# Kernel tuning notes

Measured on AMD Instinct MI355X. Metric: run time of the kernel, lower is better.

Reference implementation:

```python
import jax, jax.numpy as jnp
import numpy as np

D_MODEL = 1024
N_HEADS = 16
D_HEAD = D_MODEL // N_HEADS
MODES = 32


def setup_inputs() -> dict:
    key = jax.random.key(0)
    ks = jax.random.split(key, 7)
    B, L = 4, 4096
    s = 1.0 / np.sqrt(D_MODEL)
    return {
        "q_in": jax.random.normal(ks[0], (B, L, D_MODEL), dtype=jnp.float32),
        "Wv": jax.random.uniform(ks[1], (D_MODEL, D_MODEL), jnp.float32, -s, s),
        "bv": jax.random.uniform(ks[2], (D_MODEL,), jnp.float32, -s, s),
        "Wo": jax.random.uniform(ks[3], (D_MODEL, D_MODEL), jnp.float32, -s, s),
        "bo": jax.random.uniform(ks[4], (D_MODEL,), jnp.float32, -s, s),
        "w_real": jax.random.normal(ks[5], (N_HEADS, MODES, D_HEAD), dtype=jnp.float32) * 0.02,
        "w_imag": jax.random.normal(ks[6], (N_HEADS, MODES, D_HEAD), dtype=jnp.float32) * 0.02,
    }


def reference(q_in, Wv, bv, Wo, bo, w_real, w_imag):
    B, L, dm = q_in.shape
    # v projection -> [B, H, L, Dh]
    v = (q_in @ Wv.T + bv).reshape(B, L, N_HEADS, D_HEAD).transpose(0, 2, 1, 3)
    # rFFT over time axis; keep only lowest MODES frequencies
    v_ft = jnp.fft.rfft(v, axis=2)                      # [B, H, L//2+1, Dh] complex
    w = (w_real + 1j * w_imag)[None]                    # [1, H, MODES, Dh]
    out_ft = v_ft[:, :, :MODES, :] * w                  # truncated spectrum
    # irfft zero-pads the truncated spectrum up to n//2+1 (== torch's zeros_like + slice-assign)
    out = jnp.fft.irfft(out_ft, n=L, axis=2)            # [B, H, L, Dh]
    out = out.transpose(0, 2, 1, 3).reshape(B, L, dm)
    return out @ Wo.T + bo
```

## Files before the change

### kernel.cpp

```cpp
#include <hip/hip_runtime.h>
#include <math.h>


typedef __attribute__((ext_vector_type(8))) short bf16x8;
typedef __attribute__((ext_vector_type(8))) unsigned short ushort8;
typedef __attribute__((ext_vector_type(4))) float f32x4;

__device__ __forceinline__ unsigned short f2bf(float x) {
    union { float f; unsigned int u; } c; c.f = x;
    unsigned int u = c.u + 0x7FFFu + ((c.u >> 16) & 1u);
    return (unsigned short)(u >> 16);
}

__global__ __launch_bounds__(256) void k_init(unsigned short* __restrict__ F,
                                              unsigned short* __restrict__ G,
                                              float* __restrict__ A) {
    int idx = blockIdx.x * 256 + threadIdx.x;
    const float w0 = 1.5339807878856412e-3f;
    {
        int j = idx >> 12, t = idx & 4095, k = j >> 1;
        int r = (k * t) & 4095;
        float s, c; sincosf((float)r * w0, &s, &c);
        F[idx] = f2bf((j & 1) ? -s : c);
    }
    {
        int j = idx & 63, k = j >> 1;
        int t = idx >> 6;
        int r = (k * t) & 4095;
        float s, c; sincosf((float)r * w0, &s, &c);
        float ck = (k == 0) ? (1.0f / 4096.0f) : (2.0f / 4096.0f);
        float v = (j & 1) ? ((k == 0) ? 0.0f : -ck * s) : ck * c;
        G[idx] = f2bf(v);
    }
    A[idx] = 0.0f;
}

__global__ __launch_bounds__(64) void k_dft_fwd(const float* __restrict__ q,
                                                const unsigned short* __restrict__ F,
                                                float* __restrict__ A) {
    __shared__ __align__(16) unsigned short Ft[64 * 40];
    __shared__ __align__(16) unsigned short qT[32 * 40];
    int blk = blockIdx.x;
    int kp = blk & 15, nt = (blk >> 4) & 31, b = blk >> 9;
    int n0 = nt * 32, t0 = kp * 256;
    int lane = threadIdx.x;
    int lm = lane & 15, q4 = lane >> 4;
    int nn4 = (lane & 7) * 4, th = lane >> 3;
    f32x4 acc[4][2] = {};
    for (int ks = 0; ks < 8; ++ks) {
        int tb = t0 + ks * 32;
        #pragma unroll
        for (int i = 0; i < 4; ++i) {
            ushort8 v = *(const ushort8*)&F[lane * 4096 + tb + i * 8];
            *(ushort8*)&Ft[lane * 40 + i * 8] = v;
        }
        #pragma unroll
        for (int r2 = 0; r2 < 4; ++r2) {
            int tl = r2 * 8 + th;
            float4 v = *(const float4*)&q[(size_t)(b * 4096 + tb + tl) * 1024 + n0 + nn4];
            qT[(nn4 + 0) * 40 + tl] = f2bf(v.x);
            qT[(nn4 + 1) * 40 + tl] = f2bf(v.y);
            qT[(nn4 + 2) * 40 + tl] = f2bf(v.z);
            qT[(nn4 + 3) * 40 + tl] = f2bf(v.w);
        }
        __syncthreads();
        bf16x8 af[4], bq[2];
        #pragma unroll
        for (int mt = 0; mt < 4; ++mt)
            af[mt] = *(const bf16x8*)&Ft[(mt * 16 + lm) * 40 + q4 * 8];
        #pragma unroll
        for (int ntt = 0; ntt < 2; ++ntt)
            bq[ntt] = *(const bf16x8*)&qT[(ntt * 16 + lm) * 40 + q4 * 8];
        #pragma unroll
        for (int mt = 0; mt < 4; ++mt)
            #pragma unroll
            for (int ntt = 0; ntt < 2; ++ntt)
                acc[mt][ntt] = __builtin_amdgcn_mfma_f32_16x16x32_bf16(
                    af[mt], bq[ntt], acc[mt][ntt], 0, 0, 0);
        __syncthreads();
    }
    #pragma unroll
    for (int mt = 0; mt < 4; ++mt)
        #pragma unroll
        for (int ntt = 0; ntt < 2; ++ntt)
            #pragma unroll
            for (int r = 0; r < 4; ++r) {
                int j = mt * 16 + q4 * 4 + r;
                int n = n0 + ntt * 16 + lm;
                atomicAdd(&A[(b * 64 + j) * 1024 + n], acc[mt][ntt][r]);
            }
}

template<int ABF16>
__global__ __launch_bounds__(256) void k_gemm_bt(const void* __restrict__ Ain,
                                                 const float* __restrict__ Bmat,
                                                 float* __restrict__ P) {
    __shared__ __align__(16) unsigned short At[64 * 40];
    __shared__ __align__(16) unsigned short Wt[128 * 40];
    int blk = blockIdx.x;
    int kp = blk & 7, nt = (blk >> 3) & 7, mt = blk >> 6;
    int m0 = mt * 64, n0 = nt * 128, k0 = kp * 128;
    int tid = threadIdx.x, lane = tid & 63, w = tid >> 6;
    int lm = lane & 15, q4 = lane >> 4;
    int ma = tid >> 2, ka = (tid & 3) * 8;
    int nw = tid >> 1, kw = (tid & 1) * 16;
    f32x4 acc[4][2] = {};
    for (int ks = 0; ks < 4; ++ks) {
        int kb = k0 + ks * 32;
        if (ABF16) {
            ushort8 v = *(const ushort8*)&((const unsigned short*)Ain)[(m0 + ma) * 1024 + kb + ka];
            *(ushort8*)&At[ma * 40 + ka] = v;
        } else {
            const float* Af = (const float*)Ain;
            float4 x0 = *(const float4*)&Af[(m0 + ma) * 1024 + kb + ka];
            float4 x1 = *(const float4*)&Af[(m0 + ma) * 1024 + kb + ka + 4];
            ushort8 v;
            v[0]=f2bf(x0.x); v[1]=f2bf(x0.y); v[2]=f2bf(x0.z); v[3]=f2bf(x0.w);
            v[4]=f2bf(x1.x); v[5]=f2bf(x1.y); v[6]=f2bf(x1.z); v[7]=f2bf(x1.w);
            *(ushort8*)&At[ma * 40 + ka] = v;
        }
        {
            const float4* wp = (const float4*)&Bmat[(n0 + nw) * 1024 + kb + kw];
            float4 x0 = wp[0], x1 = wp[1], x2 = wp[2], x3 = wp[3];
            ushort8 v0, v1;
            v0[0]=f2bf(x0.x); v0[1]=f2bf(x0.y); v0[2]=f2bf(x0.z); v0[3]=f2bf(x0.w);
            v0[4]=f2bf(x1.x); v0[5]=f2bf(x1.y); v0[6]=f2bf(x1.z); v0[7]=f2bf(x1.w);
            v1[0]=f2bf(x2.x); v1[1]=f2bf(x2.y); v1[2]=f2bf(x2.z); v1[3]=f2bf(x2.w);
            v1[4]=f2bf(x3.x); v1[5]=f2bf(x3.y); v1[6]=f2bf(x3.z); v1[7]=f2bf(x3.w);
            *(ushort8*)&Wt[nw * 40 + kw]     = v0;
            *(ushort8*)&Wt[nw * 40 + kw + 8] = v1;
        }
        __syncthreads();
        bf16x8 af[4], bf[2];
        #pragma unroll
        for (int mti = 0; mti < 4; ++mti)
            af[mti] = *(const bf16x8*)&At[(mti * 16 + lm) * 40 + q4 * 8];
        #pragma unroll
        for (int ntt = 0; ntt < 2; ++ntt)
            bf[ntt] = *(const bf16x8*)&Wt[(w * 32 + ntt * 16 + lm) * 40 + q4 * 8];
        #pragma unroll
        for (int mti = 0; mti < 4; ++mti)
            #pragma unroll
            for (int ntt = 0; ntt < 2; ++ntt)
                acc[mti][ntt] = __builtin_amdgcn_mfma_f32_16x16x32_bf16(
                    af[mti], bf[ntt], acc[mti][ntt], 0, 0, 0);
        __syncthreads();
    }
    #pragma unroll
    for (int mti = 0; mti < 4; ++mti)
        #pragma unroll
        for (int ntt = 0; ntt < 2; ++ntt)
            #pragma unroll
            for (int r = 0; r < 4; ++r) {
                int m = m0 + mti * 16 + q4 * 4 + r;
                int n = n0 + w * 32 + ntt * 16 + lm;
                P[(size_t)kp * 262144 + m * 1024 + n] = acc[mti][ntt][r];
            }
}

__global__ __launch_bounds__(256) void k_cmul(const float* __restrict__ P,
                                              const float* __restrict__ bv,
                                              const float* __restrict__ wr,
                                              const float* __restrict__ wi,
                                              unsigned short* __restrict__ Y) {
    int idx = blockIdx.x * 256 + threadIdx.x;
    int n = idx & 1023, k = (idx >> 10) & 31, b = idx >> 15;
    int rowr = (b * 64 + 2 * k) * 1024 + n;
    int rowi = rowr + 1024;
    float re = 0.f, im = 0.f;
    #pragma unroll
    for (int p = 0; p < 8; ++p) {
        re += P[p * 262144 + rowr];
        im += P[p * 262144 + rowi];
    }
    if (k == 0) re += 4096.0f * bv[n];
    int h = n >> 6, dh = n & 63;
    float a = wr[(h * 32 + k) * 64 + dh];
    float c = wi[(h * 32 + k) * 64 + dh];
    Y[rowr] = f2bf(re * a - im * c);
    Y[rowi] = f2bf(re * c + im * a);
}

__global__ __launch_bounds__(256) void k_reduce8(const float* __restrict__ P,
                                                 unsigned short* __restrict__ Z) {
    int idx = blockIdx.x * 256 + threadIdx.x;
    float s = 0.f;
    #pragma unroll
    for (int p = 0; p < 8; ++p) s += P[p * 262144 + idx];
    Z[idx] = f2bf(s);
}

__global__ __launch_bounds__(256) void k_dft_inv(const unsigned short* __restrict__ G,
                                                 const unsigned short* __restrict__ Zb,
                                                 const float* __restrict__ bo,
                                                 float* __restrict__ out) {
    __shared__ __align__(16) unsigned short Gt[128 * 72];
    __shared__ __align__(16) unsigned short ZT[128 * 72];
    int blk = blockIdx.x;
    int nt = blk & 7, tt = (blk >> 3) & 31, b = blk >> 8;
    int n0 = nt * 128, t0 = tt * 128;
    int tid = threadIdx.x, lane = tid & 63, w = tid >> 6;
    int lm = lane & 15, q4 = lane >> 4;
    {
        int ttl = tid >> 1, jj = (tid & 1) * 32;
        #pragma unroll
        for (int i = 0; i < 4; ++i) {
            ushort8 v = *(const ushort8*)&G[(t0 + ttl) * 64 + jj + i * 8];
            *(ushort8*)&Gt[ttl * 72 + jj + i * 8] = v;
        }
    }
    {
        int jp = tid & 31, hi = tid >> 5;
        int j = jp * 2, nn0 = hi * 16;
        const unsigned short* r0 = &Zb[(b * 64 + j) * 1024 + n0 + nn0];
        const unsigned short* r1 = &Zb[(b * 64 + j + 1) * 1024 + n0 + nn0];
        ushort8 a0 = *(const ushort8*)r0, a1 = *(const ushort8*)(r0 + 8);
        ushort8 b0 = *(const ushort8*)r1, b1 = *(const ushort8*)(r1 + 8);
        #pragma unroll
        for (int i = 0; i < 8; ++i) {
            unsigned int v = (unsigned int)a0[i] | ((unsigned int)b0[i] << 16);
            *(unsigned int*)&ZT[(nn0 + i) * 72 + j] = v;
        }
        #pragma unroll
        for (int i = 0; i < 8; ++i) {
            unsigned int v = (unsigned int)a1[i] | ((unsigned int)b1[i] << 16);
            *(unsigned int*)&ZT[(nn0 + 8 + i) * 72 + j] = v;
        }
    }
    __syncthreads();
    int wt0 = (w >> 1) * 64, wn0 = (w & 1) * 64;
    f32x4 acc[4][4] = {};
    #pragma unroll
    for (int ks = 0; ks < 2; ++ks) {
        bf16x8 af[4], bf[4];
        #pragma unroll
        for (int mt = 0; mt < 4; ++mt)
            af[mt] = *(const bf16x8*)&Gt[(wt0 + mt * 16 + lm) * 72 + ks * 32 + q4 * 8];
        #pragma unroll
        for (int ntt = 0; ntt < 4; ++ntt)
            bf[ntt] = *(const bf16x8*)&ZT[(wn0 + ntt * 16 + lm) * 72 + ks * 32 + q4 * 8];
        #pragma unroll
        for (int mt = 0; mt < 4; ++mt)
            #pragma unroll
            for (int ntt = 0; ntt < 4; ++ntt)
                acc[mt][ntt] = __builtin_amdgcn_mfma_f32_16x16x32_bf16(
                    af[mt], bf[ntt], acc[mt][ntt], 0, 0, 0);
    }
    #pragma unroll
    for (int ntt = 0; ntt < 4; ++ntt) {
        int n = n0 + wn0 + ntt * 16 + lm;
        float bov = bo[n];
        #pragma unroll
        for (int mt = 0; mt < 4; ++mt)
            #pragma unroll
            for (int r = 0; r < 4; ++r) {
                int t = t0 + wt0 + mt * 16 + q4 * 4 + r;
                out[(size_t)(b * 4096 + t) * 1024 + n] = acc[mt][ntt][r] + bov;
            }
    }
}

extern "C" void kernel_launch(void* const* d_in, const int* in_sizes, int n_in,
                              void* d_out, int out_size, void* d_ws, size_t ws_size,
                              hipStream_t stream) {
    const float* q  = (const float*)d_in[0];
    const float* Wv = (const float*)d_in[1];
    const float* bv = (const float*)d_in[2];
    const float* Wo = (const float*)d_in[3];
    const float* bo = (const float*)d_in[4];
    const float* wr = (const float*)d_in[5];
    const float* wi = (const float*)d_in[6];
    float* out = (float*)d_out;

    char* ws = (char*)d_ws;
    unsigned short* F  = (unsigned short*)(ws);
    unsigned short* G  = (unsigned short*)(ws + (512 << 10));
    float*          A  = (float*)(ws + (1 << 20));
    unsigned short* Y  = (unsigned short*)(ws + (2 << 20));
    unsigned short* Zb = (unsigned short*)(ws + (2 << 20) + (512 << 10));
    float*          P1 = (float*)(ws + (3u << 20));
    float*          P2 = (float*)(ws + (11u << 20));

    hipLaunchKernelGGL(k_init,       dim3(1024), dim3(256), 0, stream, F, G, A);
    hipLaunchKernelGGL(k_dft_fwd,    dim3(2048), dim3(64),  0, stream, q, F, A);
    hipLaunchKernelGGL((k_gemm_bt<0>), dim3(256), dim3(256), 0, stream, (const void*)A, Wv, P1);
    hipLaunchKernelGGL(k_cmul,       dim3(512),  dim3(256), 0, stream, P1, bv, wr, wi, Y);
    hipLaunchKernelGGL((k_gemm_bt<1>), dim3(256), dim3(256), 0, stream, (const void*)Y, Wo, P2);
    hipLaunchKernelGGL(k_reduce8,    dim3(1024), dim3(256), 0, stream, P2, Zb);
    hipLaunchKernelGGL(k_dft_inv,    dim3(1024), dim3(256), 0, stream, G, Zb, bo, out);
}
```

Baseline: 170.7 us.

## Load DFT operands straight to registers and atomically reduce split-K GEMM partials

The forward DFT kernel drops its shared-memory staging and barriers. Each wave now loads F and q directly into MFMA fragment registers, converting q to bf16 in registers, using 256-thread blocks that cover 128 columns. Both split-K GEMMs now atomically accumulate into a single zeroed fp32 buffer instead of writing eight partial slices, which removes the k_reduce8 kernel and the eight-way partial reads in k_cmul. The inverse DFT reads fp32 Z and converts it to bf16 itself. The risks are uncoalesced strided q loads (eight separate rows per lane), atomic contention, and nondeterministic summation order.

```diff
diff --git a/kernel.cpp b/kernel.cpp
--- a/kernel.cpp
+++ b/kernel.cpp
@@ -14,7 +14,9 @@
 
 __global__ __launch_bounds__(256) void k_init(unsigned short* __restrict__ F,
                                               unsigned short* __restrict__ G,
-                                              float* __restrict__ A) {
+                                              float* __restrict__ A,
+                                              float* __restrict__ C,
+                                              float* __restrict__ Z) {
     int idx = blockIdx.x * 256 + threadIdx.x;
     const float w0 = 1.5339807878856412e-3f;
     {
@@ -33,51 +35,46 @@
         G[idx] = f2bf(v);
     }
     A[idx] = 0.0f;
-}
-
-__global__ __launch_bounds__(64) void k_dft_fwd(const float* __restrict__ q,
-                                                const unsigned short* __restrict__ F,
-                                                float* __restrict__ A) {
-    __shared__ __align__(16) unsigned short Ft[64 * 40];
-    __shared__ __align__(16) unsigned short qT[32 * 40];
+    C[idx] = 0.0f;
+    Z[idx] = 0.0f;
+}
+
+__global__ __launch_bounds__(256) void k_dft_fwd(const float* __restrict__ q,
+                                                 const unsigned short* __restrict__ F,
+                                                 float* __restrict__ A) {
     int blk = blockIdx.x;
-    int kp = blk & 15, nt = (blk >> 4) & 31, b = blk >> 9;
-    int n0 = nt * 32, t0 = kp * 256;
-    int lane = threadIdx.x;
+    int kp = blk & 15, nt = (blk >> 4) & 7, b = blk >> 7;
+    int tid = threadIdx.x, lane = tid & 63, w = tid >> 6;
     int lm = lane & 15, q4 = lane >> 4;
-    int nn4 = (lane & 7) * 4, th = lane >> 3;
+    int n0 = nt * 128 + w * 32;
+    int t0 = kp * 256;
     f32x4 acc[4][2] = {};
+    #pragma unroll 2
     for (int ks = 0; ks < 8; ++ks) {
-        int tb = t0 + ks * 32;
-        #pragma unroll
-        for (int i = 0; i < 4; ++i) {
-            ushort8 v = *(const ushort8*)&F[lane * 4096 + tb + i * 8];
-            *(ushort8*)&Ft[lane * 40 + i * 8] = v;
-        }
-        #pragma unroll
-        for (int r2 = 0; r2 < 4; ++r2) {
-            int tl = r2 * 8 + th;
-            float4 v = *(const float4*)&q[(size_t)(b * 4096 + tb + tl) * 1024 + n0 + nn4];
-            qT[(nn4 + 0) * 40 + tl] = f2bf(v.x);
-            qT[(nn4 + 1) * 40 + tl] = f2bf(v.y);
-            qT[(nn4 + 2) * 40 + tl] = f2bf(v.z);
-            qT[(nn4 + 3) * 40 + tl] = f2bf(v.w);
-        }
-        __syncthreads();
-        bf16x8 af[4], bq[2];
-        #pragma unroll
-        for (int mt = 0; mt < 4; ++mt)
-            af[mt] = *(const bf16x8*)&Ft[(mt * 16 + lm) * 40 + q4 * 8];
-        #pragma unroll
-        for (int ntt = 0; ntt < 2; ++ntt)
-            bq[ntt] = *(const bf16x8*)&qT[(ntt * 16 + lm) * 40 + q4 * 8];
+        int tb = t0 + ks * 32 + q4 * 8;
+        bf16x8 af[4];
+        #pragma unroll
+        for (int mt = 0; mt < 4; ++mt)
+            af[mt] = *(const bf16x8*)&F[(mt * 16 + lm) * 4096 + tb];
+        bf16x8 bq[2];
+        #pragma unroll
+        for (int ntt = 0; ntt < 2; ++ntt) {
+            const float* qp = &q[(size_t)(b * 4096 + tb) * 1024 + n0 + ntt * 16 + lm];
+            float f0 = qp[0 * 1024], f1 = qp[1 * 1024], f2 = qp[2 * 1024], f3 = qp[3 * 1024];
+            float f4 = qp[4 * 1024], f5 = qp[5 * 1024], f6 = qp[6 * 1024], f7 = qp[7 * 1024];
+            union { unsigned int u[4]; bf16x8 v; } cv;
+            cv.u[0] = (unsigned)f2bf(f0) | ((unsigned)f2bf(f1) << 16);
+            cv.u[1] = (unsigned)f2bf(f2) | ((unsigned)f2bf(f3) << 16);
+            cv.u[2] = (unsigned)f2bf(f4) | ((unsigned)f2bf(f5) << 16);
+            cv.u[3] = (unsigned)f2bf(f6) | ((unsigned)f2bf(f7) << 16);
+            bq[ntt] = cv.v;
+        }
         #pragma unroll
         for (int mt = 0; mt < 4; ++mt)
             #pragma unroll
             for (int ntt = 0; ntt < 2; ++ntt)
                 acc[mt][ntt] = __builtin_amdgcn_mfma_f32_16x16x32_bf16(
                     af[mt], bq[ntt], acc[mt][ntt], 0, 0, 0);
-        __syncthreads();
     }
     #pragma unroll
     for (int mt = 0; mt < 4; ++mt)
@@ -94,7 +91,7 @@
 template<int ABF16>
 __global__ __launch_bounds__(256) void k_gemm_bt(const void* __restrict__ Ain,
                                                  const float* __restrict__ Bmat,
-                                                 float* __restrict__ P) {
+                                                 float* __restrict__ Cout) {
     __shared__ __align__(16) unsigned short At[64 * 40];
     __shared__ __align__(16) unsigned short Wt[128 * 40];
     int blk = blockIdx.x;
@@ -154,11 +151,11 @@
             for (int r = 0; r < 4; ++r) {
                 int m = m0 + mti * 16 + q4 * 4 + r;
                 int n = n0 + w * 32 + ntt * 16 + lm;
-                P[(size_t)kp * 262144 + m * 1024 + n] = acc[mti][ntt][r];
+                atomicAdd(&Cout[m * 1024 + n], acc[mti][ntt][r]);
             }
 }
 
-__global__ __launch_bounds__(256) void k_cmul(const float* __restrict__ P,
+__global__ __launch_bounds__(256) void k_cmul(const float* __restrict__ C,
                                               const float* __restrict__ bv,
                                               const float* __restrict__ wr,
                                               const float* __restrict__ wi,
@@ -167,12 +164,8 @@
     int n = idx & 1023, k = (idx >> 10) & 31, b = idx >> 15;
     int rowr = (b * 64 + 2 * k) * 1024 + n;
     int rowi = rowr + 1024;
-    float re = 0.f, im = 0.f;
-    #pragma unroll
-    for (int p = 0; p < 8; ++p) {
-        re += P[p * 262144 + rowr];
-        im += P[p * 262144 + rowi];
-    }
+    float re = C[rowr];
+    float im = C[rowi];
     if (k == 0) re += 4096.0f * bv[n];
     int h = n >> 6, dh = n & 63;
     float a = wr[(h * 32 + k) * 64 + dh];
@@ -181,17 +174,8 @@
     Y[rowi] = f2bf(re * c + im * a);
 }
 
-__global__ __launch_bounds__(256) void k_reduce8(const float* __restrict__ P,
-                                                 unsigned short* __restrict__ Z) {
-    int idx = blockIdx.x * 256 + threadIdx.x;
-    float s = 0.f;
-    #pragma unroll
-    for (int p = 0; p < 8; ++p) s += P[p * 262144 + idx];
-    Z[idx] = f2bf(s);
-}
-
 __global__ __launch_bounds__(256) void k_dft_inv(const unsigned short* __restrict__ G,
-                                                 const unsigned short* __restrict__ Zb,
+                                                 const float* __restrict__ Zf,
                                                  const float* __restrict__ bo,
                                                  float* __restrict__ out) {
     __shared__ __align__(16) unsigned short Gt[128 * 72];
@@ -212,19 +196,20 @@
     {
         int jp = tid & 31, hi = tid >> 5;
         int j = jp * 2, nn0 = hi * 16;
-        const unsigned short* r0 = &Zb[(b * 64 + j) * 1024 + n0 + nn0];
-        const unsigned short* r1 = &Zb[(b * 64 + j + 1) * 1024 + n0 + nn0];
-        ushort8 a0 = *(const ushort8*)r0, a1 = *(const ushort8*)(r0 + 8);
-        ushort8 b0 = *(const ushort8*)r1, b1 = *(const ushort8*)(r1 + 8);
-        #pragma unroll
-        for (int i = 0; i < 8; ++i) {
-            unsigned int v = (unsigned int)a0[i] | ((unsigned int)b0[i] << 16);
+        const float* r0 = &Zf[(b * 64 + j) * 1024 + n0 + nn0];
+        const float* r1 = r0 + 1024;
+        float za[16], zb[16];
+        #pragma unroll
+        for (int i = 0; i < 4; ++i) {
+            float4 va = ((const float4*)r0)[i];
+            float4 vb = ((const float4*)r1)[i];
+            za[4*i+0] = va.x; za[4*i+1] = va.y; za[4*i+2] = va.z; za[4*i+3] = va.w;
+            zb[4*i+0] = vb.x; zb[4*i+1] = vb.y; zb[4*i+2] = vb.z; zb[4*i+3] = vb.w;
+        }
+        #pragma unroll
+        for (int i = 0; i < 16; ++i) {
+            unsigned int v = (unsigned)f2bf(za[i]) | ((unsigned)f2bf(zb[i]) << 16);
             *(unsigned int*)&ZT[(nn0 + i) * 72 + j] = v;
-        }
-        #pragma unroll
-        for (int i = 0; i < 8; ++i) {
-            unsigned int v = (unsigned int)a1[i] | ((unsigned int)b1[i] << 16);
-            *(unsigned int*)&ZT[(nn0 + 8 + i) * 72 + j] = v;
         }
     }
     __syncthreads();
@@ -275,17 +260,15 @@
     char* ws = (char*)d_ws;
     unsigned short* F  = (unsigned short*)(ws);
     unsigned short* G  = (unsigned short*)(ws + (512 << 10));
-    float*          A  = (float*)(ws + (1 << 20));
-    unsigned short* Y  = (unsigned short*)(ws + (2 << 20));
-    unsigned short* Zb = (unsigned short*)(ws + (2 << 20) + (512 << 10));
-    float*          P1 = (float*)(ws + (3u << 20));
-    float*          P2 = (float*)(ws + (11u << 20));
-
-    hipLaunchKernelGGL(k_init,       dim3(1024), dim3(256), 0, stream, F, G, A);
-    hipLaunchKernelGGL(k_dft_fwd,    dim3(2048), dim3(64),  0, stream, q, F, A);
-    hipLaunchKernelGGL((k_gemm_bt<0>), dim3(256), dim3(256), 0, stream, (const void*)A, Wv, P1);
-    hipLaunchKernelGGL(k_cmul,       dim3(512),  dim3(256), 0, stream, P1, bv, wr, wi, Y);
-    hipLaunchKernelGGL((k_gemm_bt<1>), dim3(256), dim3(256), 0, stream, (const void*)Y, Wo, P2);
-    hipLaunchKernelGGL(k_reduce8,    dim3(1024), dim3(256), 0, stream, P2, Zb);
-    hipLaunchKernelGGL(k_dft_inv,    dim3(1024), dim3(256), 0, stream, G, Zb, bo, out);
-}
+    float*          A  = (float*)(ws + (1u << 20));
+    float*          C  = (float*)(ws + (2u << 20));
+    float*          Z  = (float*)(ws + (3u << 20));
+    unsigned short* Y  = (unsigned short*)(ws + (4u << 20));
+
+    hipLaunchKernelGGL(k_init,         dim3(1024), dim3(256), 0, stream, F, G, A, C, Z);
+    hipLaunchKernelGGL(k_dft_fwd,      dim3(512),  dim3(256), 0, stream, q, F, A);
+    hipLaunchKernelGGL((k_gemm_bt<0>), dim3(256),  dim3(256), 0, stream, (const void*)A, Wv, C);
+    hipLaunchKernelGGL(k_cmul,         dim3(512),  dim3(256), 0, stream, C, bv, wr, wi, Y);
+    hipLaunchKernelGGL((k_gemm_bt<1>), dim3(256),  dim3(256), 0, stream, (const void*)Y, Wo, Z);
+    hipLaunchKernelGGL(k_dft_inv,      dim3(1024), dim3(256), 0, stream, G, Z, bo, out);
+}
```

New measurement: 175.4 us. 2.8% more time.
